# Optimization experiments

Hardware: AMD Instinct MI355X
Metric: run time of the kernel (lower is better)

Reference implementation:

```python
import jax, jax.numpy as jnp
import numpy as np

V = 512          # num vertices
F = 64           # pair-feature dim (gpnn_channels in)
C = 64           # gpnn_channels out
E = 8192         # num edges (avg degree 16)


def setup_inputs() -> dict:
    key = jax.random.key(0)
    k1, k2, k3, k4 = jax.random.split(key, 4)
    alpha = jax.random.normal(k1, (V * V, F), dtype=jnp.float32)          # pair features, row v*V+w
    edge_index = jax.random.randint(k2, (2, E), 0, V)                      # COO [src; dst]
    # GPNNEdgeConv.nn = MLP([F, C, C], act='relu')  (norm treated as identity / eval stats)
    w1 = jax.random.normal(k3, (F, C), dtype=jnp.float32) * (1.0 / np.sqrt(F))
    b1 = jnp.zeros((C,), dtype=jnp.float32)
    w2 = jax.random.normal(k4, (C, C), dtype=jnp.float32) * (1.0 / np.sqrt(C))
    b2 = jnp.zeros((C,), dtype=jnp.float32)
    eps = jnp.asarray(0.0, dtype=jnp.float32)                              # train_eps parameter
    return {"alpha": alpha, "edge_index": edge_index,
            "w1": w1, "b1": b1, "w2": w2, "b2": b2, "eps": eps}


def reference(alpha, edge_index, w1, b1, w2, b2, eps):
    # Dense 0/1 adjacency adj_t: adj[v, j] = 1 iff edge j -> v (dst-indexed, as spmm(adj_t, .)).
    adj = jnp.zeros((V, V), dtype=alpha.dtype).at[edge_index[1], edge_index[0]].set(1.0)
    a3 = alpha.reshape(V, V, F)  # a3[v, j] = alpha[v*V + j]
    # message_and_aggregate: out[v*V+w] = row v of spmm(adj_t, A_{v,w}),
    # where A_{v,w}[j] = alpha[v*V+j] + alpha[w*V+j]  (sum aggregation)
    #   = sum_j adj[v,j] * (a3[v,j] + a3[w,j]) = S[v] + T[v,w]
    S = jnp.einsum('vj,vjf->vf', adj, a3)    # [V, F]
    T = jnp.einsum('vj,wjf->vwf', adj, a3)   # [V, V, F]
    out = (S[:, None, :] + T).reshape(V * V, F)
    # GINConv residual: out + (1 + eps) * x_r, then MLP (Linear-ReLU-Linear)
    out = out + (1.0 + eps) * alpha
    h = jax.nn.relu(out @ w1 + b1)
    return h @ w2 + b2
```

## Files before the change

### kernel.cpp

```cpp
#include <hip/hip_runtime.h>
#include <hip/hip_bf16.h>

#define NV 512
#define NF 64

typedef __attribute__((ext_vector_type(8))) short bf16x8;
typedef __attribute__((ext_vector_type(4))) float f32x4;

union BF8 { bf16x8 v; unsigned u[4]; };

__device__ __forceinline__ unsigned short f2bf(float x) {
    unsigned u = __float_as_uint(x);
    unsigned r = (u + 0x7fffu + ((u >> 16) & 1u)) >> 16;
    return (unsigned short)r;
}

__device__ __forceinline__ unsigned awt_addr(int f, int jbyte) {
    return (unsigned)((f * 1024 + jbyte) ^ (((f ^ (f >> 3)) & 7) << 4));
}
__device__ __forceinline__ int slot2(int row) {
    return 2 * (((row >> 2) ^ row) & 3) + (row & 1);
}

__global__ void k_edges(const int* __restrict__ ei, int E, unsigned int* __restrict__ mask) {
    int e = blockIdx.x * 256 + threadIdx.x;
    if (e < E) {
        int s = ei[e];
        int d = ei[E + e];
        atomicOr(&mask[d * 16 + (s >> 5)], 1u << (s & 31));
    }
}

__global__ void k_S(const unsigned int* __restrict__ mask, const float* __restrict__ alpha,
                    float* __restrict__ S) {
    __shared__ float red[4][64];
    int v = blockIdx.x;
    int lane = threadIdx.x & 63;
    int g = threadIdx.x >> 6;
    float a0 = 0.f, a1 = 0.f;
    for (int wd = g * 4; wd < g * 4 + 4; ++wd) {
        unsigned bits = mask[v * 16 + wd];
        while (bits) {
            int b0 = __ffs(bits) - 1; bits &= bits - 1;
            float x0 = alpha[((size_t)v * NV + wd * 32 + b0) * NF + lane];
            if (bits) {
                int b1 = __ffs(bits) - 1; bits &= bits - 1;
                a1 += alpha[((size_t)v * NV + wd * 32 + b1) * NF + lane];
            }
            a0 += x0;
        }
    }
    red[g][lane] = a0 + a1;
    __syncthreads();
    if (g == 0)
        S[v * NF + lane] = red[0][lane] + red[1][lane] + red[2][lane] + red[3][lane];
}

__global__ __launch_bounds__(512, 2) void k_main(
    const float* __restrict__ alpha, const float* __restrict__ w1, const float* __restrict__ b1,
    const float* __restrict__ w2, const float* __restrict__ b2, const float* __restrict__ eps_p,
    const unsigned int* __restrict__ mask, const float* __restrict__ S,
    float* __restrict__ out)
{
    extern __shared__ char smem[];
    const int w    = blockIdx.x;
    const int t    = threadIdx.x;
    const int lane = t & 63;
    const int wid  = t >> 6;
    const int nlo  = lane & 15;
    const int g    = lane >> 4;
    const int kbase = g * 8;
    const int mbase = wid * 64;
    const float* src = alpha + (size_t)w * (NV * NF);

    auto stage_half = [&](int i) {
        int task = i * 512 + t;
        int jb = task >> 4;
        int fq = task & 15;
        unsigned ua[4][4];
#pragma unroll
        for (int h = 0; h < 4; ++h) {
            f32x4 r0 = *(const f32x4*)(src + (size_t)(jb * 8 + 2 * h) * NF + fq * 4);
            f32x4 r1 = *(const f32x4*)(src + (size_t)(jb * 8 + 2 * h + 1) * NF + fq * 4);
#pragma unroll
            for (int c = 0; c < 4; ++c)
                ua[c][h] = (unsigned)f2bf(r0[c]) | ((unsigned)f2bf(r1[c]) << 16);
        }
#pragma unroll
        for (int c = 0; c < 4; ++c) {
            BF8 p;
            p.u[0] = ua[c][0]; p.u[1] = ua[c][1]; p.u[2] = ua[c][2]; p.u[3] = ua[c][3];
            *(bf16x8*)(smem + awt_addr(fq * 4 + c, jb * 16)) = p.v;
        }
    };

    f32x4 acc[4][4];

    stage_half(0);

    uint4 qm[4][4];
#pragma unroll
    for (int mi = 0; mi < 4; ++mi)
#pragma unroll
        for (int kq = 0; kq < 4; ++kq)
            qm[mi][kq] = *(const uint4*)(mask + (size_t)(mbase + mi * 16 + nlo) * 16 + kq * 4);

#pragma unroll
    for (int mi = 0; mi < 4; ++mi)
#pragma unroll
        for (int nt = 0; nt < 4; ++nt)
#pragma unroll
            for (int r = 0; r < 4; ++r)
                acc[mi][nt][r] = S[(size_t)(mbase + mi * 16 + g * 4 + r) * NF + nt * 16 + nlo];

    __syncthreads();

    auto ldB = [&](int kk, bf16x8* bfr) {
#pragma unroll
        for (int nt = 0; nt < 4; ++nt)
            bfr[nt] = *(const bf16x8*)(smem + awt_addr(nt * 16 + nlo, kk * 64 + g * 16));
    };

    auto gemm_half = [&](int K0) {
        bf16x8 bfrA[4], bfrB[4];
        ldB(K0, bfrA);
#pragma unroll
        for (int kx = 0; kx < 8; ++kx) {
            const int kk = K0 + kx;
            bf16x8* cur = (kx & 1) ? bfrB : bfrA;
            bf16x8* nxt = (kx & 1) ? bfrA : bfrB;
            if (kx < 7) ldB(kk + 1, nxt);
            const int kq = kk >> 2, kr = kk & 3;
            BF8 afr[4];
#pragma unroll
            for (int mi = 0; mi < 4; ++mi) {
                unsigned byteb = ((&qm[mi][kq].x)[kr] >> (g * 8)) & 0xFFu;
#pragma unroll
                for (int h = 0; h < 4; ++h) {
                    unsigned b0 = (byteb >> (2 * h)) & 1u;
                    unsigned b1 = (byteb >> (2 * h + 1)) & 1u;
                    afr[mi].u[h] = (b0 ? 0x3F80u : 0u) | (b1 ? 0x3F800000u : 0u);
                }
            }
#pragma unroll
            for (int nt = 0; nt < 4; ++nt)
#pragma unroll
                for (int mi = 0; mi < 4; ++mi)
                    acc[mi][nt] = __builtin_amdgcn_mfma_f32_16x16x32_bf16(afr[mi].v, cur[nt], acc[mi][nt], 0, 0, 0);
        }
    };

    stage_half(1);
    gemm_half(0);
    __syncthreads();
    gemm_half(8);

    bf16x8 w1f[2][4], w2f[2][4];
#pragma unroll
    for (int ks = 0; ks < 2; ++ks)
#pragma unroll
        for (int nt = 0; nt < 4; ++nt) {
            bf16x8 a, bb;
#pragma unroll
            for (int e = 0; e < 8; ++e) {
                int k = ks * 32 + kbase + e;
                a[e]  = (short)f2bf(w1[k * NF + nt * 16 + nlo]);
                bb[e] = (short)f2bf(w2[k * NF + nt * 16 + nlo]);
            }
            w1f[ks][nt] = a;
            w2f[ks][nt] = bb;
        }
    float b1v[4], b2v[4];
#pragma unroll
    for (int nt = 0; nt < 4; ++nt) {
        b1v[nt] = b1[nt * 16 + nlo];
        b2v[nt] = b2[nt * 16 + nlo];
    }
    const float ceps = 1.0f + eps_p[0];

    __syncthreads();

    char* myscr = smem + wid * 2048;
#pragma unroll
    for (int mi = 0; mi < 4; ++mi) {
        int v0 = mbase + mi * 16;
        float rvv[4][4];
#pragma unroll
        for (int nt = 0; nt < 4; ++nt)
#pragma unroll
            for (int r = 0; r < 4; ++r)
                rvv[nt][r] = alpha[((size_t)(v0 + g * 4 + r) * NV + w) * NF + nt * 16 + nlo];
#pragma unroll
        for (int nt = 0; nt < 4; ++nt)
#pragma unroll
            for (int r = 0; r < 4; ++r) {
                float pre = acc[mi][nt][r] + ceps * rvv[nt][r];
                int row = g * 4 + r;
                *(unsigned short*)(myscr + row * 128 + ((2 * (nt * 16 + nlo)) ^ (slot2(row) << 4))) = f2bf(pre);
            }

        bf16x8 a0 = *(const bf16x8*)(myscr + nlo * 128 + ((g * 16) ^ (slot2(nlo) << 4)));
        bf16x8 a1 = *(const bf16x8*)(myscr + nlo * 128 + ((g * 16 + 64) ^ (slot2(nlo) << 4)));
        f32x4 accm[4];
#pragma unroll
        for (int nt = 0; nt < 4; ++nt) {
            f32x4 z = {0.f, 0.f, 0.f, 0.f};
            z = __builtin_amdgcn_mfma_f32_16x16x32_bf16(a0, w1f[0][nt], z, 0, 0, 0);
            z = __builtin_amdgcn_mfma_f32_16x16x32_bf16(a1, w1f[1][nt], z, 0, 0, 0);
            accm[nt] = z;
        }

#pragma unroll
        for (int nt = 0; nt < 4; ++nt)
#pragma unroll
            for (int r = 0; r < 4; ++r) {
                float hv = accm[nt][r] + b1v[nt];
                hv = hv > 0.f ? hv : 0.f;
                int row = g * 4 + r;
                *(unsigned short*)(myscr + row * 128 + ((2 * (nt * 16 + nlo)) ^ (slot2(row) << 4))) = f2bf(hv);
            }

        bf16x8 h0 = *(const bf16x8*)(myscr + nlo * 128 + ((g * 16) ^ (slot2(nlo) << 4)));
        bf16x8 h1 = *(const bf16x8*)(myscr + nlo * 128 + ((g * 16 + 64) ^ (slot2(nlo) << 4)));
#pragma unroll
        for (int nt = 0; nt < 4; ++nt) {
            f32x4 z = {0.f, 0.f, 0.f, 0.f};
            z = __builtin_amdgcn_mfma_f32_16x16x32_bf16(h0, w2f[0][nt], z, 0, 0, 0);
            z = __builtin_amdgcn_mfma_f32_16x16x32_bf16(h1, w2f[1][nt], z, 0, 0, 0);
#pragma unroll
            for (int r = 0; r < 4; ++r) {
                int vv = v0 + g * 4 + r;
                out[((size_t)vv * NV + w) * NF + nt * 16 + nlo] = z[r] + b2v[nt];
            }
        }
    }
}

extern "C" void kernel_launch(void* const* d_in, const int* in_sizes, int n_in,
                              void* d_out, int out_size, void* d_ws, size_t ws_size,
                              hipStream_t stream) {
    const float* alpha = (const float*)d_in[0];
    const int*   ei    = (const int*)d_in[1];
    const float* w1    = (const float*)d_in[2];
    const float* b1    = (const float*)d_in[3];
    const float* w2    = (const float*)d_in[4];
    const float* b2    = (const float*)d_in[5];
    const float* eps   = (const float*)d_in[6];
    float* out = (float*)d_out;
    int E = in_sizes[1] / 2;

    unsigned int* mask = (unsigned int*)d_ws;
    float* S = (float*)((char*)d_ws + 32768);

    hipMemsetAsync(mask, 0, 32768, stream);
    k_edges<<<(E + 255) / 256, 256, 0, stream>>>(ei, E, mask);
    k_S    <<<NV, 256, 0, stream>>>(mask, alpha, S);

    hipFuncSetAttribute(reinterpret_cast<const void*>(k_main),
                        hipFuncAttributeMaxDynamicSharedMemorySize, 65536);
    k_main<<<NV, 512, 65536, stream>>>(alpha, w1, b1, w2, b2, eps, mask, S, out);
}
```

Measured before the change: 68.78 us.

## Process two w columns per block with 128-row warp tiles

Each block now handles two w values, with four warps per w, and each warp computes 128 v rows instead of 64. The two staged alpha slabs live in 128KB of LDS, and mask fragments are loaded per k-quarter rather than held for the whole loop. The aim is to reuse each B fragment load across twice as many MFMAs and halve the number of blocks. In exchange, the grid drops to 256 blocks with one block per CU because of the LDS size, accumulator register pressure doubles, and the 2048-byte per-warp epilogue scratch may overlap the other w's staging region.

```diff
diff --git a/kernel.cpp b/kernel.cpp
--- a/kernel.cpp
+++ b/kernel.cpp
@@ -63,50 +63,52 @@
     float* __restrict__ out)
 {
     extern __shared__ char smem[];
-    const int w    = blockIdx.x;
+    const int bid  = blockIdx.x;
     const int t    = threadIdx.x;
     const int lane = t & 63;
     const int wid  = t >> 6;
     const int nlo  = lane & 15;
     const int g    = lane >> 4;
     const int kbase = g * 8;
-    const int mbase = wid * 64;
-    const float* src = alpha + (size_t)w * (NV * NF);
-
-    auto stage_half = [&](int i) {
-        int task = i * 512 + t;
-        int jb = task >> 4;
-        int fq = task & 15;
-        unsigned ua[4][4];
-#pragma unroll
-        for (int h = 0; h < 4; ++h) {
-            f32x4 r0 = *(const f32x4*)(src + (size_t)(jb * 8 + 2 * h) * NF + fq * 4);
-            f32x4 r1 = *(const f32x4*)(src + (size_t)(jb * 8 + 2 * h + 1) * NF + fq * 4);
-#pragma unroll
-            for (int c = 0; c < 4; ++c)
-                ua[c][h] = (unsigned)f2bf(r0[c]) | ((unsigned)f2bf(r1[c]) << 16);
-        }
-#pragma unroll
-        for (int c = 0; c < 4; ++c) {
-            BF8 p;
-            p.u[0] = ua[c][0]; p.u[1] = ua[c][1]; p.u[2] = ua[c][2]; p.u[3] = ua[c][3];
-            *(bf16x8*)(smem + awt_addr(fq * 4 + c, jb * 16)) = p.v;
+    const int wg   = wid >> 2;
+    const int wloc = wid & 3;
+    const int w    = 2 * bid + wg;
+    const int mbase = wloc * 128;
+    char* region = smem + wg * 65536;
+
+    auto stage_half = [&](int h) {
+#pragma unroll
+        for (int i = 0; i < 2; ++i) {
+            int task = i * 512 + t;
+            int wp  = task >> 9;
+            int rem = task & 511;
+            int jb  = h * 32 + (rem >> 4);
+            int fq  = rem & 15;
+            const float* srcp = alpha + (size_t)(2 * bid + wp) * (NV * NF);
+            unsigned ua[4][4];
+#pragma unroll
+            for (int hh = 0; hh < 4; ++hh) {
+                f32x4 r0 = *(const f32x4*)(srcp + (size_t)(jb * 8 + 2 * hh) * NF + fq * 4);
+                f32x4 r1 = *(const f32x4*)(srcp + (size_t)(jb * 8 + 2 * hh + 1) * NF + fq * 4);
+#pragma unroll
+                for (int c = 0; c < 4; ++c)
+                    ua[c][hh] = (unsigned)f2bf(r0[c]) | ((unsigned)f2bf(r1[c]) << 16);
+            }
+#pragma unroll
+            for (int c = 0; c < 4; ++c) {
+                BF8 p;
+                p.u[0] = ua[c][0]; p.u[1] = ua[c][1]; p.u[2] = ua[c][2]; p.u[3] = ua[c][3];
+                *(bf16x8*)(smem + wp * 65536 + awt_addr(fq * 4 + c, jb * 16)) = p.v;
+            }
         }
     };
 
-    f32x4 acc[4][4];
+    f32x4 acc[8][4];
 
     stage_half(0);
 
-    uint4 qm[4][4];
-#pragma unroll
-    for (int mi = 0; mi < 4; ++mi)
-#pragma unroll
-        for (int kq = 0; kq < 4; ++kq)
-            qm[mi][kq] = *(const uint4*)(mask + (size_t)(mbase + mi * 16 + nlo) * 16 + kq * 4);
-
-#pragma unroll
-    for (int mi = 0; mi < 4; ++mi)
+#pragma unroll
+    for (int mi = 0; mi < 8; ++mi)
 #pragma unroll
         for (int nt = 0; nt < 4; ++nt)
 #pragma unroll
@@ -115,45 +117,45 @@
 
     __syncthreads();
 
-    auto ldB = [&](int kk, bf16x8* bfr) {
-#pragma unroll
-        for (int nt = 0; nt < 4; ++nt)
-            bfr[nt] = *(const bf16x8*)(smem + awt_addr(nt * 16 + nlo, kk * 64 + g * 16));
+    auto gemm_q = [&](int kq) {
+        uint4 qm[8];
+#pragma unroll
+        for (int mi = 0; mi < 8; ++mi)
+            qm[mi] = *(const uint4*)(mask + (size_t)(mbase + mi * 16 + nlo) * 16 + kq * 4);
+#pragma unroll
+        for (int kr = 0; kr < 4; ++kr) {
+            const int kk = kq * 4 + kr;
+            bf16x8 bfr[4];
+#pragma unroll
+            for (int nt = 0; nt < 4; ++nt)
+                bfr[nt] = *(const bf16x8*)(region + awt_addr(nt * 16 + nlo, kk * 64 + g * 16));
+#pragma unroll
+            for (int mig = 0; mig < 2; ++mig) {
+                BF8 afr[4];
+#pragma unroll
+                for (int m4 = 0; m4 < 4; ++m4) {
+                    unsigned byteb = ((&qm[mig * 4 + m4].x)[kr] >> (g * 8)) & 0xFFu;
+#pragma unroll
+                    for (int h = 0; h < 4; ++h) {
+                        unsigned b0 = (byteb >> (2 * h)) & 1u;
+                        unsigned b1 = (byteb >> (2 * h + 1)) & 1u;
+                        afr[m4].u[h] = (b0 ? 0x3F80u : 0u) | (b1 ? 0x3F800000u : 0u);
+                    }
+                }
+#pragma unroll
+                for (int nt = 0; nt < 4; ++nt)
+#pragma unroll
+                    for (int m4 = 0; m4 < 4; ++m4)
+                        acc[mig * 4 + m4][nt] =
+                            __builtin_amdgcn_mfma_f32_16x16x32_bf16(afr[m4].v, bfr[nt], acc[mig * 4 + m4][nt], 0, 0, 0);
+            }
+        }
     };
 
-    auto gemm_half = [&](int K0) {
-        bf16x8 bfrA[4], bfrB[4];
-        ldB(K0, bfrA);
-#pragma unroll
-        for (int kx = 0; kx < 8; ++kx) {
-            const int kk = K0 + kx;
-            bf16x8* cur = (kx & 1) ? bfrB : bfrA;
-            bf16x8* nxt = (kx & 1) ? bfrA : bfrB;
-            if (kx < 7) ldB(kk + 1, nxt);
-            const int kq = kk >> 2, kr = kk & 3;
-            BF8 afr[4];
-#pragma unroll
-            for (int mi = 0; mi < 4; ++mi) {
-                unsigned byteb = ((&qm[mi][kq].x)[kr] >> (g * 8)) & 0xFFu;
-#pragma unroll
-                for (int h = 0; h < 4; ++h) {
-                    unsigned b0 = (byteb >> (2 * h)) & 1u;
-                    unsigned b1 = (byteb >> (2 * h + 1)) & 1u;
-                    afr[mi].u[h] = (b0 ? 0x3F80u : 0u) | (b1 ? 0x3F800000u : 0u);
-                }
-            }
-#pragma unroll
-            for (int nt = 0; nt < 4; ++nt)
-#pragma unroll
-                for (int mi = 0; mi < 4; ++mi)
-                    acc[mi][nt] = __builtin_amdgcn_mfma_f32_16x16x32_bf16(afr[mi].v, cur[nt], acc[mi][nt], 0, 0, 0);
-        }
-    };
-
     stage_half(1);
-    gemm_half(0);
-    __syncthreads();
-    gemm_half(8);
+    gemm_q(0); gemm_q(1);
+    __syncthreads();
+    gemm_q(2); gemm_q(3);
 
     bf16x8 w1f[2][4], w2f[2][4];
 #pragma unroll
@@ -182,7 +184,7 @@
 
     char* myscr = smem + wid * 2048;
 #pragma unroll
-    for (int mi = 0; mi < 4; ++mi) {
+    for (int mi = 0; mi < 8; ++mi) {
         int v0 = mbase + mi * 16;
         float rvv[4][4];
 #pragma unroll
@@ -257,6 +259,6 @@
     k_S    <<<NV, 256, 0, stream>>>(mask, alpha, S);
 
     hipFuncSetAttribute(reinterpret_cast<const void*>(k_main),
-                        hipFuncAttributeMaxDynamicSharedMemorySize, 65536);
-    k_main<<<NV, 512, 65536, stream>>>(alpha, w1, b1, w2, b2, eps, mask, S, out);
-}
+                        hipFuncAttributeMaxDynamicSharedMemorySize, 131072);
+    k_main<<<NV / 2, 512, 131072, stream>>>(alpha, w1, b1, w2, b2, eps, mask, S, out);
+}
```

After: 83.99 us. 22.1% more time.
